# Optimization experiments

Measured on AMD Instinct MI355X. Metric: run time of the kernel, lower is better.

The kernel has to match this reference:

```python
import jax, jax.numpy as jnp
import numpy as np


def _vieta_pell_basis(x, degree):
    # Iterative recurrence: V0 = 2, V1 = x, Vn = x*V_{n-1} + V_{n-2}
    basis = [2.0 * jnp.ones_like(x), x]
    for _ in range(2, degree + 1):
        basis.append(x * basis[-1] + basis[-2])
    return jnp.stack(basis[: degree + 1], axis=-1)  # [b, i, d+1]


def setup_inputs() -> dict:
    key = jax.random.key(0)
    k1, k2 = jax.random.split(key)
    batch, input_dim, output_dim, degree = 4096, 1024, 1024, 8
    x = jax.random.normal(k1, (batch, input_dim), dtype=jnp.float32)
    std = 1.0 / (input_dim * (degree + 1))
    vp_coeffs = jax.random.normal(k2, (input_dim, output_dim, degree + 1), dtype=jnp.float32) * std
    return {"x": x, "vp_coeffs": vp_coeffs}


def reference(x, vp_coeffs):
    degree = vp_coeffs.shape[-1] - 1
    xt = jnp.tanh(x)  # [b, i]
    vp_basis = _vieta_pell_basis(xt, degree)  # [b, i, d+1]
    y = jnp.einsum("bid,iod->bo", vp_basis, vp_coeffs)
    return y
```

## Files before the change

### kernel.cpp

```cpp
#include <hip/hip_runtime.h>
#include <hip/hip_bf16.h>

typedef unsigned short u16;
typedef unsigned int   u32;
typedef unsigned long long u64;

#define BATCH 4096
#define IDIM  1024
#define ODIM  1024
#define NDEG  9
#define KA    8192
#define NZ    4
#define KZ    (KA / NZ)
#define GBK   64
#define NT    (KZ / GBK)

typedef __attribute__((ext_vector_type(8))) short short8_t;
typedef __attribute__((ext_vector_type(4))) float f32x4;

__device__ __forceinline__ u16 f2bf(float f) {
    union { float f; u32 u; } v; v.f = f;
    u32 r = v.u + 0x7FFFu + ((v.u >> 16) & 1u);
    return (u16)(r >> 16);
}
__device__ __forceinline__ u32 pack2bf(float lo, float hi) {
    return (u32)f2bf(lo) | ((u32)f2bf(hi) << 16);
}
__device__ __forceinline__ float bf2f(u16 h) {
    union { u32 u; float f; } v; v.u = (u32)h << 16; return v.f;
}

__device__ __forceinline__ void gl_lds16(const u16* g, u16* l) {
    __builtin_amdgcn_global_load_lds(
        (const __attribute__((address_space(1))) void*)g,
        (__attribute__((address_space(3))) void*)l,
        16, 0, 0);
}

#define BARRIER()   __builtin_amdgcn_s_barrier()
#define WAIT_LGKM0() do { asm volatile("s_waitcnt lgkmcnt(0)" ::: "memory"); \
                          __builtin_amdgcn_sched_barrier(0); } while (0)
#define WAIT_LGKM8() asm volatile("s_waitcnt lgkmcnt(8)" ::: "memory")
#define WAIT_VM4()  asm volatile("s_waitcnt vmcnt(4)" ::: "memory")
#define WAIT_VM0()  asm volatile("s_waitcnt vmcnt(0)" ::: "memory")

#define PB_TI 128
#define PB_TO 8
#define PB_J  (PB_TO * NDEG)
#define PB_LS 132

#define NB_B   1024
#define NB_A   2048

__global__ void prep_kernel(const float* __restrict__ x,
                            const float* __restrict__ c,
                            u16* __restrict__ A, u16* __restrict__ Bt,
                            float* __restrict__ Pr) {
    __shared__ u16 lds[PB_J * PB_LS];
    const int bb  = blockIdx.x;
    const int tid = threadIdx.x;

    if (bb < NB_B) {
        const int i0 = (bb & 7) * PB_TI;
        const int o0 = (bb >> 3) * PB_TO;
        const float* src = c + (size_t)i0 * (ODIM * NDEG) + (size_t)o0 * NDEG;
#pragma unroll
        for (int t = 0; t < 36; ++t) {
            int f  = t * 256 + tid;
            int ii = f / PB_J;
            int j  = f - ii * PB_J;
            float v = src[(size_t)ii * (ODIM * NDEG) + j];
            lds[j * PB_LS + ii] = f2bf(v);
        }
        __syncthreads();

        {
            int o   = tid >> 5;
            int sub = tid & 31;
            const u16* row = lds + (o * NDEG) * PB_LS + sub * 4;
            float s = bf2f(row[0]) + bf2f(row[1]) + bf2f(row[2]) + bf2f(row[3]);
#pragma unroll
            for (int m = 16; m >= 1; m >>= 1)
                s += __shfl_xor(s, m, 64);
            if (sub == 0)
                Pr[(size_t)(bb & 7) * ODIM + o0 + o] = s;
        }

#pragma unroll
        for (int t = 0; t < 9; ++t) {
            int g   = t * 256 + tid;
            int j   = g >> 5;
            int ii4 = (g & 31) << 2;
            int o   = j / NDEG;
            int d   = j - o * NDEG;
            if (d != 0) {
                u64 v = *(const u64*)(lds + j * PB_LS + ii4);
                *(u64*)(Bt + (size_t)(o0 + o) * KA + (d - 1) * 1024 + i0 + ii4) = v;
            }
        }
    } else {
        int t  = (bb - NB_B) * 256 + tid;
        int b  = t >> 7;
        int i8 = (t & 127) << 3;
        const float4* xv = (const float4*)(x + ((size_t)t << 3));
        float4 xa = xv[0], xb = xv[1];
        float th[8] = {tanhf(xa.x), tanhf(xa.y), tanhf(xa.z), tanhf(xa.w),
                       tanhf(xb.x), tanhf(xb.y), tanhf(xb.z), tanhf(xb.w)};
        float va[8], vb[8];
#pragma unroll
        for (int j = 0; j < 8; ++j) { va[j] = 2.0f; vb[j] = th[j]; }
        u16* dst = A + (size_t)b * KA + i8;
        uint4 w;
        w.x = pack2bf(th[0], th[1]); w.y = pack2bf(th[2], th[3]);
        w.z = pack2bf(th[4], th[5]); w.w = pack2bf(th[6], th[7]);
        *(uint4*)dst = w;
#pragma unroll
        for (int d = 2; d < NDEG; ++d) {
            float nx[8];
#pragma unroll
            for (int j = 0; j < 8; ++j) {
                nx[j] = th[j] * vb[j] + va[j];
                va[j] = vb[j]; vb[j] = nx[j];
            }
            w.x = pack2bf(nx[0], nx[1]); w.y = pack2bf(nx[2], nx[3]);
            w.z = pack2bf(nx[4], nx[5]); w.w = pack2bf(nx[6], nx[7]);
            *(uint4*)(dst + (size_t)(d - 1) * 1024) = w;
        }
    }
}

__global__ __launch_bounds__(512, 2)
void gemm_kernel(const u16* __restrict__ A, const u16* __restrict__ B,
                 float* __restrict__ P, float* __restrict__ out) {
    __shared__ __align__(16) u16 ldsA[2][16384];
    __shared__ __align__(16) u16 ldsB[2][16384];

    const int tid  = threadIdx.x;
    const int lane = tid & 63;
    const int wave = tid >> 6;
    const int quad = lane >> 4;
    const int l15  = lane & 15;
    const int wm   = wave >> 2;
    const int wn   = wave & 3;

    const int bid = blockIdx.x;
    const int z   = bid >> 6;
    const int loc = bid & 63;
    const int swz = (loc & 7) * 8 + (loc >> 3);
    const int bm  = swz >> 2;
    const int bn  = swz & 3;
    const int kStart = z * KZ;

    const u16* gA[4]; const u16* gB[4];
#pragma unroll
    for (int i = 0; i < 4; ++i) {
        int s  = i * 512 + tid;
        int r  = s >> 3;
        int sc = (s & 7) ^ (r & 7);
        gA[i] = A + (size_t)(bm * 256 + r) * KA + kStart + sc * 8;
        gB[i] = B + (size_t)(bn * 256 + r) * KA + kStart + sc * 8;
    }

    f32x4 acc[8][4];
#pragma unroll
    for (int i = 0; i < 8; ++i)
#pragma unroll
        for (int j = 0; j < 4; ++j)
            acc[i][j] = (f32x4){0.f, 0.f, 0.f, 0.f};

#define STAGE_A(i, w) gl_lds16(gA[i] + (size_t)(w) * GBK, \
                               &ldsA[(w) & 1][(i) * 4096 + tid * 8])
#define STAGE_B(i, w) gl_lds16(gB[i] + (size_t)(w) * GBK, \
                               &ldsB[(w) & 1][(i) * 4096 + tid * 8])

#pragma unroll
    for (int i = 0; i < 4; ++i) { STAGE_A(i, 0); STAGE_B(i, 0); }
    STAGE_A(0, 1); STAGE_A(2, 1); STAGE_B(2, 1); STAGE_B(3, 1);
    WAIT_VM4();
    BARRIER();

    const int pc0  = quad ^ (l15 & 7);
    const int pc1  = (4 + quad) ^ (l15 & 7);
    const int rowA0 = wm * 128 + l15;
    const int rowB0 = wn * 32 + l15;

    short8_t af[4][2], bfq[2][2];

#define READ_A(lA, MH)                                                        \
    _Pragma("unroll")                                                         \
    for (int m = 0; m < 4; ++m) {                                             \
        int ro = (rowA0 + (MH) * 64 + m * 16) * 64;                           \
        af[m][0] = *(const short8_t*)((lA) + ro + pc0 * 8);                   \
        af[m][1] = *(const short8_t*)((lA) + ro + pc1 * 8);                   \
    }
#define READ_B(lB, NH)                                                        \
    _Pragma("unroll")                                                         \
    for (int n = 0; n < 2; ++n) {                                             \
        int ro = (rowB0 + (NH) * 128 + n * 16) * 64;                          \
        bfq[n][0] = *(const short8_t*)((lB) + ro + pc0 * 8);                  \
        bfq[n][1] = *(const short8_t*)((lB) + ro + pc1 * 8);                  \
    }
#define MFMA_Q(MH, NH)                                                        \
    __builtin_amdgcn_s_setprio(1);                                            \
    _Pragma("unroll")                                                         \
    for (int kk = 0; kk < 2; ++kk)                                            \
        _Pragma("unroll")                                                     \
        for (int m = 0; m < 4; ++m)                                           \
            _Pragma("unroll")                                                 \
            for (int n = 0; n < 2; ++n)                                       \
                acc[(MH) * 4 + m][(NH) * 2 + n] =                             \
                    __builtin_amdgcn_mfma_f32_16x16x32_bf16(                  \
                        af[m][kk], bfq[n][kk],                                \
                        acc[(MH) * 4 + m][(NH) * 2 + n], 0, 0, 0);            \
    __builtin_amdgcn_s_setprio(0);

    for (int t = 0; t < NT; ++t) {
        const u16* lA = ldsA[t & 1];
        const u16* lB = ldsB[t & 1];
        const bool s1 = (t + 1 < NT);
        const bool s2 = (t + 2 < NT);

        READ_A(lA, 0); READ_B(lB, 0);
        if (s1) { STAGE_A(1, t + 1); STAGE_A(3, t + 1); }
        WAIT_LGKM8();
        BARRIER();
        WAIT_LGKM0();
        MFMA_Q(0, 0);
        BARRIER();

        READ_A(lA, 0); READ_B(lB, 1);
        if (s1) { STAGE_B(0, t + 1); STAGE_B(1, t + 1); }
        WAIT_LGKM8();
        BARRIER();
        WAIT_LGKM0();
        MFMA_Q(0, 1);
        BARRIER();

        READ_A(lA, 1); READ_B(lB, 1);
        if (s2) { STAGE_A(0, t + 2); STAGE_A(2, t + 2); }
        WAIT_LGKM8();
        BARRIER();
        WAIT_LGKM0();
        MFMA_Q(1, 1);
        BARRIER();

        READ_A(lA, 1); READ_B(lB, 0);
        if (s2) { STAGE_B(2, t + 2); STAGE_B(3, t + 2); }
        WAIT_LGKM8();
        BARRIER();
        WAIT_LGKM0();
        MFMA_Q(1, 0);
        if (s2)       WAIT_VM4();
        else if (s1)  WAIT_VM0();
        BARRIER();
    }

    float* C = (z == 0) ? out : P + (size_t)(z - 1) * (BATCH * ODIM);
#pragma unroll
    for (int mh = 0; mh < 2; ++mh)
#pragma unroll
        for (int m = 0; m < 4; ++m)
#pragma unroll
            for (int nh = 0; nh < 2; ++nh)
#pragma unroll
                for (int n = 0; n < 2; ++n) {
                    int row0 = bm * 256 + wm * 128 + mh * 64 + m * 16 + quad * 4;
                    int col  = bn * 256 + nh * 128 + wn * 32 + n * 16 + l15;
#pragma unroll
                    for (int r = 0; r < 4; ++r)
                        C[(size_t)(row0 + r) * ODIM + col] = acc[mh * 4 + m][nh * 2 + n][r];
                }
}

__global__ void reduce_kernel(const float* __restrict__ P,
                              const float* __restrict__ Pr,
                              float* __restrict__ out) {
    int t  = blockIdx.x * 256 + threadIdx.x;
    int o4 = t & 255;
    f32x4 a = ((const f32x4*)out)[t];
    a += ((const f32x4*)P)[t];
    a += ((const f32x4*)(P + (size_t)BATCH * ODIM))[t];
    a += ((const f32x4*)(P + 2 * (size_t)BATCH * ODIM))[t];
    f32x4 r = (f32x4){0.f, 0.f, 0.f, 0.f};
#pragma unroll
    for (int blk = 0; blk < 8; ++blk)
        r += ((const f32x4*)Pr)[blk * 256 + o4];
    ((f32x4*)out)[t] = a + r + r;
}

extern "C" void kernel_launch(void* const* d_in, const int* in_sizes, int n_in,
                              void* d_out, int out_size, void* d_ws, size_t ws_size,
                              hipStream_t stream) {
    const float* x      = (const float*)d_in[0];
    const float* coeffs = (const float*)d_in[1];
    float* out = (float*)d_out;
    (void)ws_size;

    u16*   A  = (u16*)d_ws;
    u16*   Bt = A + (size_t)BATCH * KA;
    float* Pr = (float*)(Bt + (size_t)ODIM * KA);
    float* P  = Pr + 8 * ODIM;

    prep_kernel<<<NB_B + NB_A, 256, 0, stream>>>(x, coeffs, A, Bt, Pr);
    gemm_kernel<<<256, 512, 0, stream>>>(A, Bt, P, out);
    reduce_kernel<<<BATCH * ODIM / 1024, 256, 0, stream>>>(P, Pr, out);
}
```

Measured before the change: 200.0 us.

## Replace split-K partial buffers with atomic accumulation, fast tanh, XCD-aware tile mapping

The separate reduce pass over three split-K partial buffers is removed. An init kernel now writes the degree-0 bias term into the output, and the GEMM adds its results into the output with global float atomics. B rows are permuted so each k-step holds the A fragments while it loads fewer B fragments. The block-to-tile mapping groups blocks by XCD, and the load/wait schedule now issues six outstanding staged loads. tanhf is replaced by an exp2/rcp approximation, which costs some accuracy, and the atomic adds make the summation order nondeterministic.

```diff
diff --git a/kernel.cpp b/kernel.cpp
--- a/kernel.cpp
+++ b/kernel.cpp
@@ -30,6 +30,15 @@
     union { u32 u; float f; } v; v.u = (u32)h << 16; return v.f;
 }
 
+__device__ __forceinline__ float fast_tanh(float v) {
+    float c = fminf(fmaxf(v, -9.0f), 9.0f);
+    float u = __builtin_amdgcn_exp2f(c * 2.8853900817779268f);
+    float d = u + 1.0f;
+    float r = __builtin_amdgcn_rcpf(d);
+    r = r * (2.0f - d * r);
+    return (u - 1.0f) * r;
+}
+
 __device__ __forceinline__ void gl_lds16(const u16* g, u16* l) {
     __builtin_amdgcn_global_load_lds(
         (const __attribute__((address_space(1))) void*)g,
@@ -37,11 +46,14 @@
         16, 0, 0);
 }
 
+__device__ __forceinline__ void gatomic_fadd(float* p, float v) {
+    asm volatile("global_atomic_add_f32 %0, %1, off" :: "v"(p), "v"(v) : "memory");
+}
+
 #define BARRIER()   __builtin_amdgcn_s_barrier()
 #define WAIT_LGKM0() do { asm volatile("s_waitcnt lgkmcnt(0)" ::: "memory"); \
                           __builtin_amdgcn_sched_barrier(0); } while (0)
-#define WAIT_LGKM8() asm volatile("s_waitcnt lgkmcnt(8)" ::: "memory")
-#define WAIT_VM4()  asm volatile("s_waitcnt vmcnt(4)" ::: "memory")
+#define WAIT_VM6()  asm volatile("s_waitcnt vmcnt(6)" ::: "memory")
 #define WAIT_VM0()  asm volatile("s_waitcnt vmcnt(0)" ::: "memory")
 
 #define PB_TI 128
@@ -104,8 +116,10 @@
         int i8 = (t & 127) << 3;
         const float4* xv = (const float4*)(x + ((size_t)t << 3));
         float4 xa = xv[0], xb = xv[1];
-        float th[8] = {tanhf(xa.x), tanhf(xa.y), tanhf(xa.z), tanhf(xa.w),
-                       tanhf(xb.x), tanhf(xb.y), tanhf(xb.z), tanhf(xb.w)};
+        float th[8] = {fast_tanh(xa.x), fast_tanh(xa.y),
+                       fast_tanh(xa.z), fast_tanh(xa.w),
+                       fast_tanh(xb.x), fast_tanh(xb.y),
+                       fast_tanh(xb.z), fast_tanh(xb.w)};
         float va[8], vb[8];
 #pragma unroll
         for (int j = 0; j < 8; ++j) { va[j] = 2.0f; vb[j] = th[j]; }
@@ -129,9 +143,20 @@
     }
 }
 
+__global__ void init_kernel(const float* __restrict__ Pr,
+                            float* __restrict__ out) {
+    int t  = blockIdx.x * 256 + threadIdx.x;
+    int o4 = t & 255;
+    f32x4 r = (f32x4){0.f, 0.f, 0.f, 0.f};
+#pragma unroll
+    for (int blk = 0; blk < 8; ++blk)
+        r += ((const f32x4*)Pr)[blk * 256 + o4];
+    ((f32x4*)out)[t] = r + r;
+}
+
 __global__ __launch_bounds__(512, 2)
 void gemm_kernel(const u16* __restrict__ A, const u16* __restrict__ B,
-                 float* __restrict__ P, float* __restrict__ out) {
+                 float* __restrict__ out) {
     __shared__ __align__(16) u16 ldsA[2][16384];
     __shared__ __align__(16) u16 ldsB[2][16384];
 
@@ -144,11 +169,11 @@
     const int wn   = wave & 3;
 
     const int bid = blockIdx.x;
-    const int z   = bid >> 6;
-    const int loc = bid & 63;
-    const int swz = (loc & 7) * 8 + (loc >> 3);
-    const int bm  = swz >> 2;
-    const int bn  = swz & 3;
+    const int xcd = bid & 7;
+    const int j   = bid >> 3;
+    const int z   = j & 3;
+    const int bm  = ((xcd & 1) << 3) | (j >> 2);
+    const int bn  = xcd >> 1;
     const int kStart = z * KZ;
 
     const u16* gA[4]; const u16* gB[4];
@@ -158,15 +183,17 @@
         int r  = s >> 3;
         int sc = (s & 7) ^ (r & 7);
         gA[i] = A + (size_t)(bm * 256 + r) * KA + kStart + sc * 8;
-        gB[i] = B + (size_t)(bn * 256 + r) * KA + kStart + sc * 8;
+        int rr = r & 127, nh = r >> 7;
+        int c  = ((rr >> 5) << 6) | (rr & 31) | (nh << 5);
+        gB[i] = B + (size_t)(bn * 256 + c) * KA + kStart + sc * 8;
     }
 
     f32x4 acc[8][4];
 #pragma unroll
     for (int i = 0; i < 8; ++i)
 #pragma unroll
-        for (int j = 0; j < 4; ++j)
-            acc[i][j] = (f32x4){0.f, 0.f, 0.f, 0.f};
+        for (int jj = 0; jj < 4; ++jj)
+            acc[i][jj] = (f32x4){0.f, 0.f, 0.f, 0.f};
 
 #define STAGE_A(i, w) gl_lds16(gA[i] + (size_t)(w) * GBK, \
                                &ldsA[(w) & 1][(i) * 4096 + tid * 8])
@@ -175,43 +202,45 @@
 
 #pragma unroll
     for (int i = 0; i < 4; ++i) { STAGE_A(i, 0); STAGE_B(i, 0); }
-    STAGE_A(0, 1); STAGE_A(2, 1); STAGE_B(2, 1); STAGE_B(3, 1);
-    WAIT_VM4();
+    STAGE_A(0, 1); STAGE_A(2, 1);
+    STAGE_B(2, 1); STAGE_B(3, 1);
+    STAGE_A(1, 1); STAGE_A(3, 1);
+    WAIT_VM6();
     BARRIER();
 
-    const int pc0  = quad ^ (l15 & 7);
-    const int pc1  = (4 + quad) ^ (l15 & 7);
-    const int rowA0 = wm * 128 + l15;
-    const int rowB0 = wn * 32 + l15;
+    const int pc0   = (quad ^ (l15 & 7)) * 8;
+    const int pc1   = (((4 + quad) ^ (l15 & 7))) * 8;
+    const int baseA = (wm * 128 + l15) * 64;
+    const int baseB = (wn * 32 + l15) * 64;
 
     short8_t af[4][2], bfq[2][2];
 
 #define READ_A(lA, MH)                                                        \
     _Pragma("unroll")                                                         \
-    for (int m = 0; m < 4; ++m) {                                             \
-        int ro = (rowA0 + (MH) * 64 + m * 16) * 64;                           \
-        af[m][0] = *(const short8_t*)((lA) + ro + pc0 * 8);                   \
-        af[m][1] = *(const short8_t*)((lA) + ro + pc1 * 8);                   \
+    for (int mt = 0; mt < 4; ++mt) {                                          \
+        int ro = baseA + (MH) * 4096 + mt * 1024;                             \
+        af[mt][0] = *(const short8_t*)((lA) + ro + pc0);                      \
+        af[mt][1] = *(const short8_t*)((lA) + ro + pc1);                      \
     }
 #define READ_B(lB, NH)                                                        \
     _Pragma("unroll")                                                         \
     for (int n = 0; n < 2; ++n) {                                             \
-        int ro = (rowB0 + (NH) * 128 + n * 16) * 64;                          \
-        bfq[n][0] = *(const short8_t*)((lB) + ro + pc0 * 8);                  \
-        bfq[n][1] = *(const short8_t*)((lB) + ro + pc1 * 8);                  \
+        int ro = baseB + (NH) * 8192 + n * 1024;                              \
+        bfq[n][0] = *(const short8_t*)((lB) + ro + pc0);                      \
+        bfq[n][1] = *(const short8_t*)((lB) + ro + pc1);                      \
     }
 #define MFMA_Q(MH, NH)                                                        \
     __builtin_amdgcn_s_setprio(1);                                            \
     _Pragma("unroll")                                                         \
     for (int kk = 0; kk < 2; ++kk)                                            \
         _Pragma("unroll")                                                     \
-        for (int m = 0; m < 4; ++m)                                           \
+        for (int mt = 0; mt < 4; ++mt)                                        \
             _Pragma("unroll")                                                 \
             for (int n = 0; n < 2; ++n)                                       \
-                acc[(MH) * 4 + m][(NH) * 2 + n] =                             \
+                acc[(MH) * 4 + mt][(NH) * 2 + n] =                            \
                     __builtin_amdgcn_mfma_f32_16x16x32_bf16(                  \
-                        af[m][kk], bfq[n][kk],                                \
-                        acc[(MH) * 4 + m][(NH) * 2 + n], 0, 0, 0);            \
+                        af[mt][kk], bfq[n][kk],                               \
+                        acc[(MH) * 4 + mt][(NH) * 2 + n], 0, 0, 0);           \
     __builtin_amdgcn_s_setprio(0);
 
     for (int t = 0; t < NT; ++t) {
@@ -221,71 +250,50 @@
         const bool s2 = (t + 2 < NT);
 
         READ_A(lA, 0); READ_B(lB, 0);
-        if (s1) { STAGE_A(1, t + 1); STAGE_A(3, t + 1); }
-        WAIT_LGKM8();
+        if (s1) { STAGE_B(0, t + 1); STAGE_B(1, t + 1); }
         BARRIER();
         WAIT_LGKM0();
         MFMA_Q(0, 0);
         BARRIER();
 
-        READ_A(lA, 0); READ_B(lB, 1);
-        if (s1) { STAGE_B(0, t + 1); STAGE_B(1, t + 1); }
-        WAIT_LGKM8();
+        READ_B(lB, 1);
+        if (s2) { STAGE_A(0, t + 2); STAGE_A(2, t + 2); }
         BARRIER();
         WAIT_LGKM0();
         MFMA_Q(0, 1);
         BARRIER();
 
-        READ_A(lA, 1); READ_B(lB, 1);
-        if (s2) { STAGE_A(0, t + 2); STAGE_A(2, t + 2); }
-        WAIT_LGKM8();
+        READ_A(lA, 1);
+        if (s2) { STAGE_B(2, t + 2); STAGE_B(3, t + 2); }
         BARRIER();
         WAIT_LGKM0();
         MFMA_Q(1, 1);
         BARRIER();
 
-        READ_A(lA, 1); READ_B(lB, 0);
-        if (s2) { STAGE_B(2, t + 2); STAGE_B(3, t + 2); }
-        WAIT_LGKM8();
+        READ_B(lB, 0);
+        if (s2) { STAGE_A(1, t + 2); STAGE_A(3, t + 2); }
         BARRIER();
         WAIT_LGKM0();
         MFMA_Q(1, 0);
-        if (s2)       WAIT_VM4();
-        else if (s1)  WAIT_VM0();
-        BARRIER();
-    }
-
-    float* C = (z == 0) ? out : P + (size_t)(z - 1) * (BATCH * ODIM);
+        if (s2) WAIT_VM6(); else WAIT_VM0();
+        BARRIER();
+    }
+
 #pragma unroll
     for (int mh = 0; mh < 2; ++mh)
 #pragma unroll
-        for (int m = 0; m < 4; ++m)
+        for (int mt = 0; mt < 4; ++mt)
 #pragma unroll
             for (int nh = 0; nh < 2; ++nh)
 #pragma unroll
                 for (int n = 0; n < 2; ++n) {
-                    int row0 = bm * 256 + wm * 128 + mh * 64 + m * 16 + quad * 4;
-                    int col  = bn * 256 + nh * 128 + wn * 32 + n * 16 + l15;
+                    int row0 = bm * 256 + wm * 128 + mh * 64 + mt * 16 + quad * 4;
+                    int col  = bn * 256 + wn * 64 + nh * 32 + n * 16 + l15;
 #pragma unroll
                     for (int r = 0; r < 4; ++r)
-                        C[(size_t)(row0 + r) * ODIM + col] = acc[mh * 4 + m][nh * 2 + n][r];
+                        gatomic_fadd(out + (size_t)(row0 + r) * ODIM + col,
+                                     acc[mh * 4 + mt][nh * 2 + n][r]);
                 }
-}
-
-__global__ void reduce_kernel(const float* __restrict__ P,
-                              const float* __restrict__ Pr,
-                              float* __restrict__ out) {
-    int t  = blockIdx.x * 256 + threadIdx.x;
-    int o4 = t & 255;
-    f32x4 a = ((const f32x4*)out)[t];
-    a += ((const f32x4*)P)[t];
-    a += ((const f32x4*)(P + (size_t)BATCH * ODIM))[t];
-    a += ((const f32x4*)(P + 2 * (size_t)BATCH * ODIM))[t];
-    f32x4 r = (f32x4){0.f, 0.f, 0.f, 0.f};
-#pragma unroll
-    for (int blk = 0; blk < 8; ++blk)
-        r += ((const f32x4*)Pr)[blk * 256 + o4];
-    ((f32x4*)out)[t] = a + r + r;
 }
 
 extern "C" void kernel_launch(void* const* d_in, const int* in_sizes, int n_in,
@@ -299,9 +307,8 @@
     u16*   A  = (u16*)d_ws;
     u16*   Bt = A + (size_t)BATCH * KA;
     float* Pr = (float*)(Bt + (size_t)ODIM * KA);
-    float* P  = Pr + 8 * ODIM;
 
     prep_kernel<<<NB_B + NB_A, 256, 0, stream>>>(x, coeffs, A, Bt, Pr);
-    gemm_kernel<<<256, 512, 0, stream>>>(A, Bt, P, out);
-    reduce_kernel<<<BATCH * ODIM / 1024, 256, 0, stream>>>(P, Pr, out);
-}
+    init_kernel<<<BATCH * ODIM / 1024, 256, 0, stream>>>(Pr, out);
+    gemm_kernel<<<256, 512, 0, stream>>>(A, Bt, out);
+}
```

Result: slower. 222.9 us (+11.5%).
